# Optimization experiments

Hardware: AMD Instinct MI355X
Metric: run time of the kernel (lower is better)

Reference implementation:

```python
import jax, jax.numpy as jnp
import numpy as np

D_MODEL = 1024
NUM_HEADS = 16
D_K = D_MODEL // NUM_HEADS
ROPE_THETA = 10000.0


def apply_rope(x, positions):
    # x: (b, h, s, d_k), positions: (b, s) int
    half = D_K // 2
    inv_freq = ROPE_THETA ** (-jnp.arange(half, dtype=jnp.float32) * 2.0 / D_K)  # (half,)
    angles = positions[:, None, :, None].astype(jnp.float32) * inv_freq  # (b,1,s,half)
    cos, sin = jnp.cos(angles), jnp.sin(angles)
    x_even = x[..., 0::2]
    x_odd = x[..., 1::2]
    r_even = x_even * cos - x_odd * sin
    r_odd = x_even * sin + x_odd * cos
    # re-interleave
    out = jnp.stack([r_even, r_odd], axis=-1).reshape(x.shape)
    return out


def setup_inputs() -> dict:
    key = jax.random.key(0)
    k1, k2, k3, k4, k5 = jax.random.split(key, 5)
    b, s = 2, 2048
    scale = 1.0 / np.sqrt(D_MODEL)
    x = jax.random.normal(k1, (b, s, D_MODEL), dtype=jnp.float32)
    w_q = jax.random.normal(k2, (D_MODEL, D_MODEL), dtype=jnp.float32) * scale
    w_k = jax.random.normal(k3, (D_MODEL, D_MODEL), dtype=jnp.float32) * scale
    w_v = jax.random.normal(k4, (D_MODEL, D_MODEL), dtype=jnp.float32) * scale
    w_o = jax.random.normal(k5, (D_MODEL, D_MODEL), dtype=jnp.float32) * scale
    token_positions = jnp.broadcast_to(jnp.arange(s, dtype=jnp.int64 if jax.config.jax_enable_x64 else jnp.int32), (b, s))
    return {"x": x, "w_q": w_q, "w_k": w_k, "w_v": w_v, "w_o": w_o,
            "token_positions": token_positions}


def reference(x, w_q, w_k, w_v, w_o, token_positions):
    b, s, _ = x.shape
    # QKV projections: w_* are (h*d_k, d_model); y = x @ w^T
    def proj(w):
        y = jnp.einsum('bsd,ed->bse', x, w)  # (b,s,h*d_k)
        return y.reshape(b, s, NUM_HEADS, D_K).transpose(0, 2, 1, 3)  # (b,h,s,d_k)
    Q, K, V = proj(w_q), proj(w_k), proj(w_v)
    Q = apply_rope(Q, token_positions)
    K = apply_rope(K, token_positions)
    scores = jnp.einsum('bhqd,bhkd->bhqk', Q, K) / jnp.sqrt(jnp.float32(D_K))
    causal = jnp.tril(jnp.ones((s, s), dtype=bool))
    scores = jnp.where(causal[None, None], scores, -jnp.inf)
    attn = jax.nn.softmax(scores, axis=-1)
    out = jnp.einsum('bhqk,bhkd->bhqd', attn, V)  # (b,h,s,d_v)
    out = out.transpose(0, 2, 1, 3).reshape(b, s, NUM_HEADS * D_K)
    return jnp.einsum('bse,de->bsd', out, w_o)
```

## Files before the change

### kernel.cpp

```cpp
#include <hip/hip_runtime.h>

#define B_ 2
#define S_ 2048
#define DM 1024
#define NH 16
#define DK 64

using bf16x8  = __attribute__((ext_vector_type(8)))  short;
using f32x4   = __attribute__((ext_vector_type(4)))  float;

__device__ __forceinline__ float bf2f(short v){
  unsigned u = ((unsigned)(unsigned short)v) << 16;
  union { unsigned u; float f; } c; c.u = u; return c.f;
}
__device__ __forceinline__ short f2bf(float f){
  union { float f; unsigned u; } c; c.f = f;
  unsigned u = c.u + 0x7FFFu + ((c.u >> 16) & 1u);
  return (short)(u >> 16);
}
__device__ __forceinline__ unsigned packbf(float lo, float hi){
  union { float f; unsigned u; } a, b; a.f = lo; b.f = hi;
  return __builtin_amdgcn_perm(b.u, a.u, 0x07060302u);
}
__device__ __forceinline__ void gload16(const void* g, void* l){
  __builtin_amdgcn_global_load_lds(
    (const __attribute__((address_space(1))) unsigned*)g,
    (__attribute__((address_space(3))) unsigned*)l, 16, 0, 0);
}

__global__ void rope_table(const int* __restrict__ pos, float* __restrict__ tab){
  int idx = blockIdx.x * blockDim.x + threadIdx.x;
  if (idx >= B_ * S_ * 32) return;
  int j = idx & 31, bs = idx >> 5;
  float p = (float)pos[bs];
  float inv = powf(10000.0f, -(float)(2 * j) / 64.0f);
  float ang = p * inv;
  tab[(size_t)bs * 64 + j]      = cosf(ang);
  tab[(size_t)bs * 64 + 32 + j] = sinf(ang);
}

__global__ void cast_all(const float* __restrict__ x, const float* __restrict__ wq,
                         const float* __restrict__ wk, const float* __restrict__ wv,
                         const float* __restrict__ wo,
                         short* __restrict__ xb, short* __restrict__ wqkv,
                         short* __restrict__ wob){
  int i = blockIdx.x * blockDim.x + threadIdx.x;
  const float4* src; short4* dst;
  if (i < (1 << 20)){
    src = (const float4*)x + i; dst = (short4*)xb + i;
  } else {
    int j = i - (1 << 20);
    int seg = j >> 18, off = j & ((1 << 18) - 1);
    const float* sp = seg == 0 ? wq : seg == 1 ? wk : seg == 2 ? wv : wo;
    short* dp = seg < 3 ? wqkv + ((size_t)seg << 20) : wob;
    src = (const float4*)sp + off; dst = (short4*)dp + off;
  }
  float4 v = *src;
  short4 o; o.x = f2bf(v.x); o.y = f2bf(v.y); o.z = f2bf(v.z); o.w = f2bf(v.w);
  *dst = o;
}

template<typename OutT>
__launch_bounds__(512)
__global__ void gemm_bt8(const short* __restrict__ A, const short* __restrict__ Bm,
                         OutT* __restrict__ C, int M, int N, int K){
  __shared__ short As[128 * 32];
  __shared__ short Bs[128 * 32];
  const int tid = threadIdx.x;
  const int l = tid & 63, w = tid >> 6;
  const int lr = l & 15, lg = l >> 4;
  const int wr = w >> 2, wc = w & 3;
  const int nwg = gridDim.x * gridDim.y;
  const int wg  = blockIdx.y * gridDim.x + blockIdx.x;
  const int sw  = (wg & 7) * (nwg >> 3) + (wg >> 3);
  const int bn  = sw % gridDim.x, bm = sw / gridDim.x;
  const short* Ab = A + (size_t)bm * 128 * K;
  const short* Bb = Bm + (size_t)bn * 128 * K;
  f32x4 acc[4][2];
  #pragma unroll
  for (int m = 0; m < 4; ++m)
    #pragma unroll
    for (int n = 0; n < 2; ++n) acc[m][n] = (f32x4){0.f, 0.f, 0.f, 0.f};
  const int r0 = tid >> 2, q4 = tid & 3;
  for (int kt = 0; kt < K; kt += 32){
    gload16(Ab + (size_t)r0 * K + kt + q4 * 8, As + tid * 8);
    gload16(Bb + (size_t)r0 * K + kt + q4 * 8, Bs + tid * 8);
    __syncthreads();
    bf16x8 a[4], bfr[2];
    #pragma unroll
    for (int m = 0; m < 4; ++m)
      a[m] = *(const bf16x8*)(As + (wr * 64 + m * 16 + lr) * 32 + lg * 8);
    #pragma unroll
    for (int n = 0; n < 2; ++n)
      bfr[n] = *(const bf16x8*)(Bs + (wc * 32 + n * 16 + lr) * 32 + lg * 8);
    #pragma unroll
    for (int m = 0; m < 4; ++m)
      #pragma unroll
      for (int n = 0; n < 2; ++n)
        acc[m][n] = __builtin_amdgcn_mfma_f32_16x16x32_bf16(a[m], bfr[n], acc[m][n], 0, 0, 0);
    __syncthreads();
  }
  #pragma unroll
  for (int m = 0; m < 4; ++m)
    #pragma unroll
    for (int n = 0; n < 2; ++n)
      #pragma unroll
      for (int j = 0; j < 4; ++j){
        int row = bm * 128 + wr * 64 + m * 16 + lg * 4 + j;
        int col = bn * 128 + wc * 32 + n * 16 + lr;
        float v = acc[m][n][j];
        if constexpr (__is_same(OutT, short)) C[(size_t)row * N + col] = f2bf(v);
        else                                  C[(size_t)row * N + col] = v;
      }
}

__global__ void rope_reshape(const short* __restrict__ qkv, const float* __restrict__ tab,
                             short* __restrict__ Qr, short* __restrict__ Kr){
  int idx = blockIdx.x * blockDim.x + threadIdx.x;
  int which = idx >> 21;
  int p = idx & ((1 << 21) - 1);
  int dp = p & 31;
  int h  = (p >> 5) & 15;
  int bs = p >> 9;
  const short* src = qkv + (size_t)bs * 3072 + which * 1024 + h * 64 + dp * 2;
  int pk = *(const int*)src;
  float e = bf2f((short)(pk & 0xFFFF));
  float o = bf2f((short)((unsigned)pk >> 16));
  const float* tb = tab + (size_t)bs * 64;
  float c = tb[dp], s = tb[32 + dp];
  float re = e * c - o * s;
  float ro = e * s + o * c;
  if (which == 0){ re *= 0.125f; ro *= 0.125f; }
  unsigned pack = (unsigned)(unsigned short)f2bf(re) | ((unsigned)(unsigned short)f2bf(ro) << 16);
  int b = bs >> 11, si = bs & 2047;
  int* dstbase = (int*)(which ? Kr : Qr);
  dstbase[((size_t)(b * NH + h) * S_ + si) * 32 + dp] = pack;
}

__global__ void vtrans(const short* __restrict__ qkv, short* __restrict__ Vt){
  __shared__ short t[64][72];
  const int tid = threadIdx.x;
  const int st = blockIdx.x, bh = blockIdx.y;
  const int b = bh >> 4, h = bh & 15;
  #pragma unroll
  for (int i = 0; i < 2; ++i){
    int c = tid + 256 * i;
    int sl = c >> 3, d8 = c & 7;
    const short* src = qkv + ((size_t)b * S_ + st * 64 + sl) * 3072 + 2048 + h * 64 + d8 * 8;
    *(bf16x8*)(&t[sl][d8 * 8]) = *(const bf16x8*)src;
  }
  __syncthreads();
  #pragma unroll
  for (int i = 0; i < 2; ++i){
    int c = tid + 256 * i;
    int dl = c >> 3, s8 = c & 7;
    bf16x8 v;
    #pragma unroll
    for (int jj = 0; jj < 8; ++jj) v[jj] = t[s8 * 8 + jj][dl];
    short* dst = Vt + ((size_t)bh * DK + dl) * S_ + st * 64 + s8 * 8;
    *(bf16x8*)dst = v;
  }
}

__device__ __forceinline__ void attn_tile_step(
    const bf16x8 qa0, const bf16x8 qa1,
    f32x4 (&acc)[4], float& mrow, float& lsum,
    const short* Ks, const short* Vs, unsigned* pw,
    int diagmask, int lr, int lg, int wl){
  float sv[4][4];
  #pragma unroll
  for (int n = 0; n < 4; ++n){
    const int R = n * 16 + lr;
    const int c0 = lg ^ (R & 7);
    bf16x8 k0 = *(const bf16x8*)(Ks + R * 64 + c0 * 8);
    bf16x8 k1 = *(const bf16x8*)(Ks + R * 64 + (c0 ^ 4) * 8);
    f32x4 z = (f32x4){0.f, 0.f, 0.f, 0.f};
    z = __builtin_amdgcn_mfma_f32_16x16x32_bf16(k0, qa0, z, 0, 0, 0);
    z = __builtin_amdgcn_mfma_f32_16x16x32_bf16(k1, qa1, z, 0, 0, 0);
    #pragma unroll
    for (int j = 0; j < 4; ++j) sv[n][j] = z[j];
  }
  if (diagmask){
    const int qloc = wl * 16 + lr;
    #pragma unroll
    for (int n = 0; n < 4; ++n)
      #pragma unroll
      for (int j = 0; j < 4; ++j)
        if (n * 16 + lg * 4 + j > qloc) sv[n][j] = -1e30f;
  }
  float lm = sv[0][0];
  #pragma unroll
  for (int n = 0; n < 4; ++n)
    #pragma unroll
    for (int j = 0; j < 4; ++j) lm = fmaxf(lm, sv[n][j]);
  lm = fmaxf(lm, __shfl_xor(lm, 16));
  lm = fmaxf(lm, __shfl_xor(lm, 32));
  if (!__all(lm <= mrow + 8.f)){
    float mnew = fmaxf(mrow, lm);
    float corr = __expf(mrow - mnew);
    mrow = mnew;
    lsum *= corr;
    float cb[4];
    #pragma unroll
    for (int j = 0; j < 4; ++j) cb[j] = __shfl(corr, lg * 4 + j);
    #pragma unroll
    for (int n = 0; n < 4; ++n)
      #pragma unroll
      for (int j = 0; j < 4; ++j) acc[n][j] *= cb[j];
  }
  float psum = 0.f;
  #pragma unroll
  for (int n = 0; n < 4; ++n)
    #pragma unroll
    for (int j = 0; j < 4; ++j){
      float p = __expf(sv[n][j] - mrow);
      sv[n][j] = p; psum += p;
    }
  psum += __shfl_xor(psum, 16);
  psum += __shfl_xor(psum, 32);
  lsum += psum;
  const int swz = (lr & 7) << 2;
  #pragma unroll
  for (int n = 0; n < 4; ++n){
    pw[lr * 32 + ((n * 8 + lg * 2 + 0) ^ swz)] = packbf(sv[n][0], sv[n][1]);
    pw[lr * 32 + ((n * 8 + lg * 2 + 1) ^ swz)] = packbf(sv[n][2], sv[n][3]);
  }
  bf16x8 pa0 = *(const bf16x8*)(pw + lr * 32 + ((lg * 4) ^ swz));
  bf16x8 pa1 = *(const bf16x8*)(pw + lr * 32 + ((16 + lg * 4) ^ swz));
  #pragma unroll
  for (int n = 0; n < 4; ++n){
    const int R = n * 16 + lr;
    const int c0 = lg ^ (R & 7);
    bf16x8 v0 = *(const bf16x8*)(Vs + R * 64 + c0 * 8);
    bf16x8 v1 = *(const bf16x8*)(Vs + R * 64 + (c0 ^ 4) * 8);
    acc[n] = __builtin_amdgcn_mfma_f32_16x16x32_bf16(pa0, v0, acc[n], 0, 0, 0);
    acc[n] = __builtin_amdgcn_mfma_f32_16x16x32_bf16(pa1, v1, acc[n], 0, 0, 0);
  }
}

__launch_bounds__(512)
__global__ void attn_kernel(const short* __restrict__ Qr, const short* __restrict__ Kr,
                            const short* __restrict__ Vt, short* __restrict__ AO){
  __shared__ short Ks[2][64 * 64];
  __shared__ short Vs[2][64 * 64];
  __shared__ unsigned Pw[8][16 * 32];
  const int tid = threadIdx.x;
  const int l = tid & 63, w = tid >> 6;
  const int lr = l & 15, lg = l >> 4;
  const int wl = w & 3, wgp = w >> 2;
  const int qp = blockIdx.x, h = blockIdx.y, b = blockIdx.z;
  const int t0 = qp, t1 = 31 - qp;
  const int myqt = wgp ? t0 : t1;
  const int bh = b * NH + h;
  const short* Qp = Qr + (size_t)bh * S_ * DK;
  const short* Kp = Kr + (size_t)bh * S_ * DK;
  const short* Vp = Vt + (size_t)bh * DK * S_;

  bf16x8 qa0, qa1;
  {
    const short* q0 = Qp + (size_t)(myqt * 64 + wl * 16 + lr) * DK + lg * 8;
    qa0 = *(const bf16x8*)q0; qa1 = *(const bf16x8*)(q0 + 32);
  }
  f32x4 acc[4];
  float ms = -1e30f, ls = 0.f;
  #pragma unroll
  for (int n = 0; n < 4; ++n) acc[n] = (f32x4){0.f, 0.f, 0.f, 0.f};
  unsigned* pw = &Pw[w][0];
  const int r0 = tid >> 3, q8 = tid & 7;
  const int sq8 = q8 ^ (r0 & 7);

  gload16(Kp + (size_t)r0 * DK + sq8 * 8, &Ks[0][tid * 8]);
  gload16(Vp + (size_t)r0 * S_ + sq8 * 8, &Vs[0][tid * 8]);
  int cur = 0;
  for (int kt = 0; kt <= t1; ++kt){
    __syncthreads();
    if (kt < t1){
      gload16(Kp + (size_t)((kt + 1) * 64 + r0) * DK + sq8 * 8, &Ks[cur ^ 1][tid * 8]);
      gload16(Vp + (size_t)r0 * S_ + (kt + 1) * 64 + sq8 * 8,   &Vs[cur ^ 1][tid * 8]);
    }
    if (kt <= myqt)
      attn_tile_step(qa0, qa1, acc, ms, ls, Ks[cur], Vs[cur], pw, kt == myqt, lr, lg, wl);
    cur ^= 1;
  }
  const float li = 1.f / ls;
  #pragma unroll
  for (int j = 0; j < 4; ++j){
    const float d0 = __shfl(li, lg * 4 + j);
    #pragma unroll
    for (int n = 0; n < 4; ++n){
      int e = h * 64 + n * 16 + lr;
      int r = myqt * 64 + wl * 16 + lg * 4 + j;
      AO[((size_t)b * S_ + r) * DM + e] = f2bf(acc[n][j] * d0);
    }
  }
}

extern "C" void kernel_launch(void* const* d_in, const int* in_sizes, int n_in,
                              void* d_out, int out_size, void* d_ws, size_t ws_size,
                              hipStream_t stream){
  const float* x  = (const float*)d_in[0];
  const float* wq = (const float*)d_in[1];
  const float* wk = (const float*)d_in[2];
  const float* wv = (const float*)d_in[3];
  const float* wo = (const float*)d_in[4];
  const int*  pos = (const int*)d_in[5];

  char* ws = (char*)d_ws;
  short* xb   = (short*)(ws + 0);
  short* wqkv = (short*)(ws + ((size_t)8  << 20));
  short* wob  = (short*)(ws + ((size_t)14 << 20));
  short* qkv  = (short*)(ws + ((size_t)16 << 20));
  short* Qr   = (short*)(ws + ((size_t)40 << 20));
  short* Kr   = (short*)(ws + ((size_t)48 << 20));
  short* Vt   = (short*)(ws + ((size_t)56 << 20));
  float* tab  = (float*)(ws + ((size_t)64 << 20));
  short* AO   = xb;
  float* out  = (float*)d_out;

  rope_table<<<dim3((B_ * S_ * 32 + 255) / 256), dim3(256), 0, stream>>>(pos, tab);
  cast_all<<<dim3(8192), dim3(256), 0, stream>>>(x, wq, wk, wv, wo, xb, wqkv, wob);
  gemm_bt8<short><<<dim3(24, 32), dim3(512), 0, stream>>>(xb, wqkv, qkv, 4096, 3072, 1024);
  rope_reshape<<<dim3(16384), dim3(256), 0, stream>>>(qkv, tab, Qr, Kr);
  vtrans<<<dim3(32, 32), dim3(256), 0, stream>>>(qkv, Vt);
  attn_kernel<<<dim3(16, NH, B_), dim3(512), 0, stream>>>(Qr, Kr, Vt, AO);
  gemm_bt8<float><<<dim3(8, 32), dim3(512), 0, stream>>>(AO, wob, out, 4096, 1024, 1024);
}
```

Baseline: 134.2 us.

## Rewrite attention inner step with 32x32x16 MFMA and register-only P exchange

Switches the attention kernel from 16x16x32 MFMA tiles to 32x32x16 tiles, so each wave owns 32 query rows and the block shrinks from 8 waves to 4. The softmax probabilities are repacked into MFMA operand layout with cross-lane shuffles instead of a round trip through LDS, which drops the per-wave P buffer. Row max and sum reductions need one shuffle instead of two, and the output is written as packed 8-byte stores. Fewer waves per block may reduce latency hiding, and the larger accumulators raise register pressure.

```diff
diff --git a/kernel.cpp b/kernel.cpp
--- a/kernel.cpp
+++ b/kernel.cpp
@@ -8,6 +8,7 @@
 
 using bf16x8  = __attribute__((ext_vector_type(8)))  short;
 using f32x4   = __attribute__((ext_vector_type(4)))  float;
+using f32x16  = __attribute__((ext_vector_type(16))) float;
 
 __device__ __forceinline__ float bf2f(short v){
   unsigned u = ((unsigned)(unsigned short)v) << 16;
@@ -22,10 +23,16 @@
   union { float f; unsigned u; } a, b; a.f = lo; b.f = hi;
   return __builtin_amdgcn_perm(b.u, a.u, 0x07060302u);
 }
+__device__ __forceinline__ unsigned pack2(float a, float b){
+  return (unsigned)(unsigned short)f2bf(a) | ((unsigned)(unsigned short)f2bf(b) << 16);
+}
 __device__ __forceinline__ void gload16(const void* g, void* l){
   __builtin_amdgcn_global_load_lds(
     (const __attribute__((address_space(1))) unsigned*)g,
     (__attribute__((address_space(3))) unsigned*)l, 16, 0, 0);
+}
+__device__ __forceinline__ f32x16 mfma32(bf16x8 a, bf16x8 b, f32x16 c){
+  return __builtin_amdgcn_mfma_f32_32x32x16_bf16(a, b, c, 0, 0, 0);
 }
 
 __global__ void rope_table(const int* __restrict__ pos, float* __restrict__ tab){
@@ -162,92 +169,90 @@
   }
 }
 
-__device__ __forceinline__ void attn_tile_step(
-    const bf16x8 qa0, const bf16x8 qa1,
-    f32x4 (&acc)[4], float& mrow, float& lsum,
-    const short* Ks, const short* Vs, unsigned* pw,
-    int diagmask, int lr, int lg, int wl){
-  float sv[4][4];
-  #pragma unroll
-  for (int n = 0; n < 4; ++n){
-    const int R = n * 16 + lr;
-    const int c0 = lg ^ (R & 7);
-    bf16x8 k0 = *(const bf16x8*)(Ks + R * 64 + c0 * 8);
-    bf16x8 k1 = *(const bf16x8*)(Ks + R * 64 + (c0 ^ 4) * 8);
-    f32x4 z = (f32x4){0.f, 0.f, 0.f, 0.f};
-    z = __builtin_amdgcn_mfma_f32_16x16x32_bf16(k0, qa0, z, 0, 0, 0);
-    z = __builtin_amdgcn_mfma_f32_16x16x32_bf16(k1, qa1, z, 0, 0, 0);
-    #pragma unroll
-    for (int j = 0; j < 4; ++j) sv[n][j] = z[j];
-  }
+__device__ __forceinline__ void attn_step32(
+    const bf16x8 (&qb)[4], f32x16& acc0, f32x16& acc1,
+    float& mrow, float& lsum,
+    const short* Ksb, const short* Vsb,
+    int diagmask, int l31, int hi, int wl){
+  f32x16 z0, z1;
+  #pragma unroll
+  for (int i = 0; i < 16; ++i){ z0[i] = 0.f; z1[i] = 0.f; }
+  const int rsw = l31 & 7;
+  #pragma unroll
+  for (int ds = 0; ds < 4; ++ds){
+    const int slot = (ds * 2 + hi) ^ rsw;
+    bf16x8 k0 = *(const bf16x8*)(Ksb + l31 * 64        + slot * 8);
+    bf16x8 k1 = *(const bf16x8*)(Ksb + (32 + l31) * 64 + slot * 8);
+    z0 = mfma32(k0, qb[ds], z0);
+    z1 = mfma32(k1, qb[ds], z1);
+  }
+  float sv[32];
+  #pragma unroll
+  for (int r = 0; r < 16; ++r){ sv[r] = z0[r]; sv[16 + r] = z1[r]; }
   if (diagmask){
-    const int qloc = wl * 16 + lr;
-    #pragma unroll
-    for (int n = 0; n < 4; ++n)
+    const int qloc = wl * 32 + l31;
+    #pragma unroll
+    for (int t2 = 0; t2 < 2; ++t2)
       #pragma unroll
-      for (int j = 0; j < 4; ++j)
-        if (n * 16 + lg * 4 + j > qloc) sv[n][j] = -1e30f;
-  }
-  float lm = sv[0][0];
-  #pragma unroll
-  for (int n = 0; n < 4; ++n)
-    #pragma unroll
-    for (int j = 0; j < 4; ++j) lm = fmaxf(lm, sv[n][j]);
-  lm = fmaxf(lm, __shfl_xor(lm, 16));
+      for (int r = 0; r < 16; ++r){
+        const int kloc = t2 * 32 + (r & 3) + 8 * (r >> 2) + 4 * hi;
+        if (kloc > qloc) sv[t2 * 16 + r] = -1e30f;
+      }
+  }
+  float lm = sv[0];
+  #pragma unroll
+  for (int i = 1; i < 32; ++i) lm = fmaxf(lm, sv[i]);
   lm = fmaxf(lm, __shfl_xor(lm, 32));
   if (!__all(lm <= mrow + 8.f)){
-    float mnew = fmaxf(mrow, lm);
-    float corr = __expf(mrow - mnew);
-    mrow = mnew;
-    lsum *= corr;
-    float cb[4];
-    #pragma unroll
-    for (int j = 0; j < 4; ++j) cb[j] = __shfl(corr, lg * 4 + j);
-    #pragma unroll
-    for (int n = 0; n < 4; ++n)
-      #pragma unroll
-      for (int j = 0; j < 4; ++j) acc[n][j] *= cb[j];
-  }
-  float psum = 0.f;
-  #pragma unroll
-  for (int n = 0; n < 4; ++n)
-    #pragma unroll
-    for (int j = 0; j < 4; ++j){
-      float p = __expf(sv[n][j] - mrow);
-      sv[n][j] = p; psum += p;
-    }
-  psum += __shfl_xor(psum, 16);
-  psum += __shfl_xor(psum, 32);
-  lsum += psum;
-  const int swz = (lr & 7) << 2;
-  #pragma unroll
-  for (int n = 0; n < 4; ++n){
-    pw[lr * 32 + ((n * 8 + lg * 2 + 0) ^ swz)] = packbf(sv[n][0], sv[n][1]);
-    pw[lr * 32 + ((n * 8 + lg * 2 + 1) ^ swz)] = packbf(sv[n][2], sv[n][3]);
-  }
-  bf16x8 pa0 = *(const bf16x8*)(pw + lr * 32 + ((lg * 4) ^ swz));
-  bf16x8 pa1 = *(const bf16x8*)(pw + lr * 32 + ((16 + lg * 4) ^ swz));
-  #pragma unroll
-  for (int n = 0; n < 4; ++n){
-    const int R = n * 16 + lr;
-    const int c0 = lg ^ (R & 7);
-    bf16x8 v0 = *(const bf16x8*)(Vs + R * 64 + c0 * 8);
-    bf16x8 v1 = *(const bf16x8*)(Vs + R * 64 + (c0 ^ 4) * 8);
-    acc[n] = __builtin_amdgcn_mfma_f32_16x16x32_bf16(pa0, v0, acc[n], 0, 0, 0);
-    acc[n] = __builtin_amdgcn_mfma_f32_16x16x32_bf16(pa1, v1, acc[n], 0, 0, 0);
-  }
-}
-
-__launch_bounds__(512)
+    const float mnew = fmaxf(mrow, lm);
+    const float corr = __expf(mrow - mnew);
+    mrow = mnew; lsum *= corr;
+    #pragma unroll
+    for (int i = 0; i < 16; ++i){ acc0[i] *= corr; acc1[i] *= corr; }
+  }
+  float ps = 0.f;
+  #pragma unroll
+  for (int i = 0; i < 32; ++i){
+    const float e = __expf(sv[i] - mrow);
+    sv[i] = e; ps += e;
+  }
+  ps += __shfl_xor(ps, 32);
+  lsum += ps;
+  unsigned p0[8], p1[8];
+  #pragma unroll
+  for (int bb = 0; bb < 8; ++bb){
+    const int i0 = (bb >> 2) * 16 + (bb & 3) * 4;
+    p0[bb] = packbf(sv[i0 + 0], sv[i0 + 1]);
+    p1[bb] = packbf(sv[i0 + 2], sv[i0 + 3]);
+  }
+  #pragma unroll
+  for (int ks = 0; ks < 4; ++ks){
+    const unsigned s0 = hi ? p0[2 * ks] : p0[2 * ks + 1];
+    const unsigned s1 = hi ? p1[2 * ks] : p1[2 * ks + 1];
+    const unsigned r0e = __shfl_xor(s0, 32);
+    const unsigned r1e = __shfl_xor(s1, 32);
+    union { unsigned u[4]; bf16x8 v; } pf;
+    pf.u[0] = hi ? r0e          : p0[2 * ks];
+    pf.u[1] = hi ? r1e          : p1[2 * ks];
+    pf.u[2] = hi ? p0[2 * ks+1] : r0e;
+    pf.u[3] = hi ? p1[2 * ks+1] : r1e;
+    const int slot = (ks * 2 + hi) ^ rsw;
+    bf16x8 v0 = *(const bf16x8*)(Vsb + l31 * 64        + slot * 8);
+    bf16x8 v1 = *(const bf16x8*)(Vsb + (32 + l31) * 64 + slot * 8);
+    acc0 = mfma32(v0, pf.v, acc0);
+    acc1 = mfma32(v1, pf.v, acc1);
+  }
+}
+
+__launch_bounds__(256)
 __global__ void attn_kernel(const short* __restrict__ Qr, const short* __restrict__ Kr,
                             const short* __restrict__ Vt, short* __restrict__ AO){
   __shared__ short Ks[2][64 * 64];
   __shared__ short Vs[2][64 * 64];
-  __shared__ unsigned Pw[8][16 * 32];
   const int tid = threadIdx.x;
   const int l = tid & 63, w = tid >> 6;
-  const int lr = l & 15, lg = l >> 4;
-  const int wl = w & 3, wgp = w >> 2;
+  const int l31 = l & 31, hi = l >> 5;
+  const int wl = w & 1, wgp = w >> 1;
   const int qp = blockIdx.x, h = blockIdx.y, b = blockIdx.z;
   const int t0 = qp, t1 = 31 - qp;
   const int myqt = wgp ? t0 : t1;
@@ -256,41 +261,58 @@
   const short* Kp = Kr + (size_t)bh * S_ * DK;
   const short* Vp = Vt + (size_t)bh * DK * S_;
 
-  bf16x8 qa0, qa1;
+  bf16x8 qb[4];
   {
-    const short* q0 = Qp + (size_t)(myqt * 64 + wl * 16 + lr) * DK + lg * 8;
-    qa0 = *(const bf16x8*)q0; qa1 = *(const bf16x8*)(q0 + 32);
-  }
-  f32x4 acc[4];
+    const short* qrow = Qp + (size_t)(myqt * 64 + wl * 32 + l31) * DK;
+    #pragma unroll
+    for (int ds = 0; ds < 4; ++ds) qb[ds] = *(const bf16x8*)(qrow + (ds * 2 + hi) * 8);
+  }
+  f32x16 acc0, acc1;
+  #pragma unroll
+  for (int i = 0; i < 16; ++i){ acc0[i] = 0.f; acc1[i] = 0.f; }
   float ms = -1e30f, ls = 0.f;
-  #pragma unroll
-  for (int n = 0; n < 4; ++n) acc[n] = (f32x4){0.f, 0.f, 0.f, 0.f};
-  unsigned* pw = &Pw[w][0];
-  const int r0 = tid >> 3, q8 = tid & 7;
-  const int sq8 = q8 ^ (r0 & 7);
-
-  gload16(Kp + (size_t)r0 * DK + sq8 * 8, &Ks[0][tid * 8]);
-  gload16(Vp + (size_t)r0 * S_ + sq8 * 8, &Vs[0][tid * 8]);
+
+  const int r0 = tid >> 3, c8 = tid & 7;
+  const int sc = c8 ^ (r0 & 7);
+  {
+    const short* kb = Kp + (size_t)r0 * DK + sc * 8;
+    gload16(kb,           &Ks[0][tid * 8]);
+    gload16(kb + 32 * DK, &Ks[0][(tid + 256) * 8]);
+    const short* vb = Vp + (size_t)r0 * S_ + sc * 8;
+    gload16(vb,           &Vs[0][tid * 8]);
+    gload16(vb + 32 * S_, &Vs[0][(tid + 256) * 8]);
+  }
   int cur = 0;
   for (int kt = 0; kt <= t1; ++kt){
     __syncthreads();
     if (kt < t1){
-      gload16(Kp + (size_t)((kt + 1) * 64 + r0) * DK + sq8 * 8, &Ks[cur ^ 1][tid * 8]);
-      gload16(Vp + (size_t)r0 * S_ + (kt + 1) * 64 + sq8 * 8,   &Vs[cur ^ 1][tid * 8]);
+      const short* kb = Kp + (size_t)((kt + 1) * 64 + r0) * DK + sc * 8;
+      gload16(kb,           &Ks[cur ^ 1][tid * 8]);
+      gload16(kb + 32 * DK, &Ks[cur ^ 1][(tid + 256) * 8]);
+      const short* vb = Vp + (size_t)r0 * S_ + (kt + 1) * 64 + sc * 8;
+      gload16(vb,           &Vs[cur ^ 1][tid * 8]);
+      gload16(vb + 32 * S_, &Vs[cur ^ 1][(tid + 256) * 8]);
     }
     if (kt <= myqt)
-      attn_tile_step(qa0, qa1, acc, ms, ls, Ks[cur], Vs[cur], pw, kt == myqt, lr, lg, wl);
+      attn_step32(qb, acc0, acc1, ms, ls, Ks[cur], Vs[cur], kt == myqt, l31, hi, wl);
     cur ^= 1;
   }
   const float li = 1.f / ls;
-  #pragma unroll
-  for (int j = 0; j < 4; ++j){
-    const float d0 = __shfl(li, lg * 4 + j);
-    #pragma unroll
-    for (int n = 0; n < 4; ++n){
-      int e = h * 64 + n * 16 + lr;
-      int r = myqt * 64 + wl * 16 + lg * 4 + j;
-      AO[((size_t)b * S_ + r) * DM + e] = f2bf(acc[n][j] * d0);
+  const int qrow = myqt * 64 + wl * 32 + l31;
+  short* dst = AO + ((size_t)b * S_ + qrow) * DM + h * 64;
+  #pragma unroll
+  for (int g = 0; g < 4; ++g){
+    {
+      uint2 st;
+      st.x = pack2(acc0[g * 4 + 0] * li, acc0[g * 4 + 1] * li);
+      st.y = pack2(acc0[g * 4 + 2] * li, acc0[g * 4 + 3] * li);
+      *(uint2*)(dst + 8 * g + 4 * hi) = st;
+    }
+    {
+      uint2 st;
+      st.x = pack2(acc1[g * 4 + 0] * li, acc1[g * 4 + 1] * li);
+      st.y = pack2(acc1[g * 4 + 2] * li, acc1[g * 4 + 3] * li);
+      *(uint2*)(dst + 32 + 8 * g + 4 * hi) = st;
     }
   }
 }
@@ -322,6 +344,6 @@
   gemm_bt8<short><<<dim3(24, 32), dim3(512), 0, stream>>>(xb, wqkv, qkv, 4096, 3072, 1024);
   rope_reshape<<<dim3(16384), dim3(256), 0, stream>>>(qkv, tab, Qr, Kr);
   vtrans<<<dim3(32, 32), dim3(256), 0, stream>>>(qkv, Vt);
-  attn_kernel<<<dim3(16, NH, B_), dim3(512), 0, stream>>>(Qr, Kr, Vt, AO);
+  attn_kernel<<<dim3(16, NH, B_), dim3(256), 0, stream>>>(Qr, Kr, Vt, AO);
   gemm_bt8<float><<<dim3(8, 32), dim3(512), 0, stream>>>(AO, wob, out, 4096, 1024, 1024);
 }
```

Measured after the change: 148.0 us. 10.3% more time.
